# Kernel tuning notes

Hardware: AMD Instinct MI355X
Metric: run time of the kernel (lower is better)

## Reference

```python
import jax, jax.numpy as jnp
import numpy as np


def setup_inputs() -> dict:
    key = jax.random.key(0)
    k1, k2 = jax.random.split(key)
    B, T, D = 32, 512, 256
    x = jax.random.normal(k1, (B, T, D), dtype=jnp.float32)
    x_pred_dur = jax.random.randint(k2, (B, T), 0, 8, dtype=jnp.int32)
    return {"x": x, "x_pred_dur": x_pred_dur, "max_dur": 4096}


def reference(x, x_pred_dur, max_dur):
    # x: [B, T, D] float phoneme features; x_pred_dur: [B, T] int frame counts.
    # Equivalent to repeat_interleave along T per batch, padded to max_dur.
    B, T, D = x.shape
    cum = jnp.cumsum(x_pred_dur, axis=1)              # [B, T] exclusive-end offsets
    total = cum[:, -1]                                # [B] mel lengths
    frames = jnp.arange(max_dur, dtype=cum.dtype)     # [M]
    # For each output frame j, the source phoneme is the first t with cum[t] > j.
    idx = jax.vmap(lambda c: jnp.searchsorted(c, frames, side='right'))(cum)  # [B, M]
    idx = jnp.minimum(idx, T - 1)                     # clamp out-of-range (padding region)
    out = jnp.take_along_axis(x, idx[..., None], axis=1)     # [B, M, D] gather
    valid = (frames[None, :] < total[:, None])[..., None]    # [B, M, 1]
    out = jnp.where(valid, out, jnp.zeros((), dtype=x.dtype))
    return out, total.astype(jnp.int32)
```

## Files before the change

kernel.cpp:

```cpp
#include <hip/hip_runtime.h>

#define BB 32
#define TT 512
#define DD 256
#define MAXDUR 4096
#define D4 (DD / 4)
#define FPB 64

__global__ __launch_bounds__(TT)
void lr_scan_kernel(const int* __restrict__ dur,
                    int* __restrict__ cum,
                    float* __restrict__ out_total) {
    __shared__ int s[TT];
    const int b = blockIdx.x;
    const int t = threadIdx.x;
    s[t] = dur[b * TT + t];
    __syncthreads();
    #pragma unroll
    for (int off = 1; off < TT; off <<= 1) {
        int v = (t >= off) ? s[t - off] : 0;
        __syncthreads();
        s[t] += v;
        __syncthreads();
    }
    cum[b * TT + t] = s[t];
    if (t == TT - 1) {
        out_total[b] = (float)s[t];
    }
}

__global__ __launch_bounds__(256)
void lr_gather_kernel(const float* __restrict__ x,
                      const int* __restrict__ cum,
                      float* __restrict__ out) {
    __shared__ int scum[TT];
    __shared__ int sidx[FPB];

    const int blocksPerBatch = MAXDUR / FPB;
    const int b = blockIdx.x / blocksPerBatch;
    const int chunk = blockIdx.x % blocksPerBatch;
    const int f0 = chunk * FPB;
    const int tid = threadIdx.x;

    #pragma unroll
    for (int i = tid; i < TT; i += 256) scum[i] = cum[b * TT + i];
    __syncthreads();

    const int total = scum[TT - 1];

    if (tid < FPB) {
        const int f = f0 + tid;
        int lo = 0, hi = TT;
        #pragma unroll
        for (int it = 0; it < 9; ++it) {
            int mid = (lo + hi) >> 1;
            if (lo < hi) {
                if (scum[mid] <= f) lo = mid + 1; else hi = mid;
            }
        }
        int idx = lo < TT - 1 ? lo : TT - 1;
        sidx[tid] = (f < total) ? idx : -1;
    }
    __syncthreads();

    const int vec = tid & 63;
    const int fl  = tid >> 6;
    const float4* __restrict__ x4 = (const float4*)x;
    float4* __restrict__ out4 = (float4*)out;
    const float4 zero = make_float4(0.f, 0.f, 0.f, 0.f);

    #pragma unroll
    for (int it = 0; it < FPB / 4; ++it) {
        const int flocal = it * 4 + fl;
        const int f = f0 + flocal;
        const int idx = sidx[flocal];
        float4 v = zero;
        if (idx >= 0) {
            v = x4[((size_t)b * TT + idx) * D4 + vec];
        }
        out4[((size_t)b * MAXDUR + f) * D4 + vec] = v;
    }
}

extern "C" void kernel_launch(void* const* d_in, const int* in_sizes, int n_in,
                              void* d_out, int out_size, void* d_ws, size_t ws_size,
                              hipStream_t stream) {
    const float* x   = (const float*)d_in[0];
    const int*   dur = (const int*)d_in[1];

    float* out = (float*)d_out;
    float* out_total = out + (size_t)BB * MAXDUR * DD;
    int* cum = (int*)d_ws;

    lr_scan_kernel<<<BB, TT, 0, stream>>>(dur, cum, out_total);
    lr_gather_kernel<<<BB * (MAXDUR / FPB), 256, 0, stream>>>(x, cum, out);
}
```

Measured before the change: 32.23 us.

## Fuse duration prefix-scan into gather kernel, removing separate scan launch

Removes the separate scan kernel and its workspace round-trip. Each gather block now computes the prefix sum of its batch's durations in shared memory, with two elements per thread and a 256-wide Hillis-Steele scan. This drops one kernel launch and the dependency between the two kernels. The cost is that the scan work is repeated in every one of the 64 blocks per batch, adding about eight barrier rounds per block before the gather begins.

```diff
diff --git a/kernel.cpp b/kernel.cpp
--- a/kernel.cpp
+++ b/kernel.cpp
@@ -7,33 +7,13 @@
 #define D4 (DD / 4)
 #define FPB 64
 
-__global__ __launch_bounds__(TT)
-void lr_scan_kernel(const int* __restrict__ dur,
-                    int* __restrict__ cum,
-                    float* __restrict__ out_total) {
-    __shared__ int s[TT];
-    const int b = blockIdx.x;
-    const int t = threadIdx.x;
-    s[t] = dur[b * TT + t];
-    __syncthreads();
-    #pragma unroll
-    for (int off = 1; off < TT; off <<= 1) {
-        int v = (t >= off) ? s[t - off] : 0;
-        __syncthreads();
-        s[t] += v;
-        __syncthreads();
-    }
-    cum[b * TT + t] = s[t];
-    if (t == TT - 1) {
-        out_total[b] = (float)s[t];
-    }
-}
-
 __global__ __launch_bounds__(256)
-void lr_gather_kernel(const float* __restrict__ x,
-                      const int* __restrict__ cum,
-                      float* __restrict__ out) {
+void lr_fused_kernel(const float* __restrict__ x,
+                     const int* __restrict__ dur,
+                     float* __restrict__ out,
+                     float* __restrict__ out_total) {
     __shared__ int scum[TT];
+    __shared__ int sp[256];
     __shared__ int sidx[FPB];
 
     const int blocksPerBatch = MAXDUR / FPB;
@@ -42,11 +22,27 @@
     const int f0 = chunk * FPB;
     const int tid = threadIdx.x;
 
+    int2 d2 = ((const int2*)(dur + b * TT))[tid];
+    const int a0 = d2.x;
+    const int a1 = d2.x + d2.y;
+    sp[tid] = a1;
+    __syncthreads();
     #pragma unroll
-    for (int i = tid; i < TT; i += 256) scum[i] = cum[b * TT + i];
+    for (int off = 1; off < 256; off <<= 1) {
+        int v = (tid >= off) ? sp[tid - off] : 0;
+        __syncthreads();
+        sp[tid] += v;
+        __syncthreads();
+    }
+    const int off_excl = sp[tid] - a1;
+    scum[2 * tid]     = off_excl + a0;
+    scum[2 * tid + 1] = off_excl + a1;
     __syncthreads();
 
     const int total = scum[TT - 1];
+    if (chunk == 0 && tid == 0) {
+        out_total[b] = (float)total;
+    }
 
     if (tid < FPB) {
         const int f = f0 + tid;
@@ -90,8 +86,6 @@
 
     float* out = (float*)d_out;
     float* out_total = out + (size_t)BB * MAXDUR * DD;
-    int* cum = (int*)d_ws;
 
-    lr_scan_kernel<<<BB, TT, 0, stream>>>(dur, cum, out_total);
-    lr_gather_kernel<<<BB * (MAXDUR / FPB), 256, 0, stream>>>(x, cum, out);
+    lr_fused_kernel<<<BB * (MAXDUR / FPB), 256, 0, stream>>>(x, dur, out, out_total);
 }
```

Result: faster. 28.12 us (-12.8%).
